# Kernel tuning notes

Measured on AMD Instinct MI355X. Metric: run time of the kernel, lower is better.

The kernel has to match this reference:

```python
import jax, jax.numpy as jnp
import numpy as np

N_HEAD = 16

def _rope(t, cos, sin):
    # t: [B,T,H,hd]; cos/sin: [T, hd//2]
    B, T, H, hd = t.shape
    tr = t.reshape(B, T, H, hd // 2, 2)
    t0, t1 = tr[..., 0], tr[..., 1]
    c = cos[None, :T, None, :]
    s = sin[None, :T, None, :]
    out = jnp.stack([t0 * c - t1 * s, t0 * s + t1 * c], axis=-1)
    return out.reshape(B, T, H, hd)

def setup_inputs() -> dict:
    key = jax.random.key(0)
    B, T, D = 2, 2048, 1024
    hd = D // N_HEAD
    ks = jax.random.split(key, 5)
    x = jax.random.normal(ks[0], (B, T, D), dtype=jnp.float32)
    Wq = jax.random.normal(ks[1], (D, D), dtype=jnp.float32) * 0.02
    Wk = jax.random.normal(ks[2], (D, D), dtype=jnp.float32) * 0.02
    Wv = jax.random.normal(ks[3], (D, D), dtype=jnp.float32) * 0.02
    Wo = jax.random.normal(ks[4], (D, D), dtype=jnp.float32) * 0.02
    # Real rotary tables (cos/sin of theta-based angles), matching precompute_freqs_cis
    theta = 10000.0
    inv_freq = 1.0 / (theta ** (np.arange(0, hd, 2, dtype=np.float32) / hd))
    ang = np.outer(np.arange(T, dtype=np.float32), inv_freq)  # [T, hd//2]
    freqs_cos = jnp.asarray(np.cos(ang), dtype=jnp.float32)
    freqs_sin = jnp.asarray(np.sin(ang), dtype=jnp.float32)
    return {"x": x, "Wq": Wq, "Wk": Wk, "Wv": Wv, "Wo": Wo,
            "freqs_cos": freqs_cos, "freqs_sin": freqs_sin}

def reference(x, Wq, Wk, Wv, Wo, freqs_cos, freqs_sin):
    B, T, D = x.shape
    H = N_HEAD
    hd = D // H
    scale = hd ** -0.5
    q = (x @ Wq.T).reshape(B, T, H, hd)
    k = (x @ Wk.T).reshape(B, T, H, hd)
    v = (x @ Wv.T).reshape(B, T, H, hd)
    q = _rope(q, freqs_cos, freqs_sin)
    k = _rope(k, freqs_cos, freqs_sin)
    # scores: [B,H,T,T]
    scores = jnp.einsum('bqhd,bkhd->bhqk', q, k) * scale
    causal = jnp.tril(jnp.ones((T, T), dtype=bool))
    scores = jnp.where(causal[None, None], scores, -jnp.inf)
    attn = jax.nn.softmax(scores, axis=-1)
    out = jnp.einsum('bhqk,bkhd->bqhd', attn, v).reshape(B, T, D)
    return out @ Wo.T
```

## Files before the change

kernel.cpp:

```cpp
#include <hip/hip_runtime.h>
#include <math.h>

typedef __bf16 bf16;
typedef __bf16 bf16x8 __attribute__((ext_vector_type(8)));
typedef __bf16 bf16x4 __attribute__((ext_vector_type(4)));
typedef __bf16 bf16x2 __attribute__((ext_vector_type(2)));
typedef float  f32x4  __attribute__((ext_vector_type(4)));

#define B_DIM 2
#define T_LEN 2048
#define D_DIM 1024
#define N_HEAD 16
#define HEAD_D 64
#define M_ROWS (B_DIM * T_LEN)

#define GLDS16(g, l)                                                          \
    __builtin_amdgcn_global_load_lds(                                         \
        (const __attribute__((address_space(1))) void*)(g),                   \
        (__attribute__((address_space(3))) void*)(l), 16, 0, 0)

__global__ void prep_cvt(const float* __restrict__ x, const float* __restrict__ wq,
                         const float* __restrict__ wk, const float* __restrict__ wv,
                         const float* __restrict__ wo, bf16* __restrict__ xb,
                         bf16* __restrict__ wqkv, bf16* __restrict__ wob) {
    int id = blockIdx.x * blockDim.x + threadIdx.x;
    if (id >= (1 << 21)) return;
    const float* src; bf16* dst; int off;
    if (id < (1 << 20)) { src = x; dst = xb; off = id; }
    else {
        int r = id - (1 << 20);
        int wi = r >> 18;
        off = r & ((1 << 18) - 1);
        src = wi == 0 ? wq : wi == 1 ? wk : wi == 2 ? wv : wo;
        dst = wi < 3 ? wqkv + ((size_t)wi << 20) : wob;
    }
    float4 v = reinterpret_cast<const float4*>(src)[off];
    bf16x4 w;
    w[0] = (bf16)v.x; w[1] = (bf16)v.y; w[2] = (bf16)v.z; w[3] = (bf16)v.w;
    reinterpret_cast<bf16x4*>(dst)[off] = w;
}

template <int MODE>
__global__ __launch_bounds__(256)
void gemm_glds(const bf16* __restrict__ A, const bf16* __restrict__ Bm,
               bf16* __restrict__ q, bf16* __restrict__ k, bf16* __restrict__ v,
               float* __restrict__ outf) {
    constexpr int K = D_DIM;
    __shared__ bf16 As[128 * 64];
    __shared__ bf16 Bs[128 * 64];
    const int tid = threadIdx.x, lane = tid & 63, wave = tid >> 6;
    const int wr = wave >> 1, wc = wave & 1;
    const int rowg = lane >> 4, col0 = lane & 15;

    const int nwg = gridDim.x * gridDim.y, cpx = nwg >> 3;
    const int lin = blockIdx.x + blockIdx.y * gridDim.x;
    const int nid = (lin & 7) * cpx + (lin >> 3);
    const int bx = nid % gridDim.x, by = nid / gridDim.x;
    const int m0 = by * 128, n0 = bx * 128;

    const int srow = lane >> 3;
    const int schk = (lane & 7) ^ srow;
    const bf16* gA = A + (size_t)(m0 + wave * 32 + srow) * K + schk * 8;
    const bf16* gB = Bm + (size_t)(n0 + wave * 32 + srow) * K + schk * 8;

    f32x4 acc[4][4];
    f32x4 zero = {0.f, 0.f, 0.f, 0.f};
#pragma unroll
    for (int i = 0; i < 4; i++)
#pragma unroll
        for (int j = 0; j < 4; j++) acc[i][j] = zero;

    for (int k0 = 0; k0 < K; k0 += 64) {
#pragma unroll
        for (int t = 0; t < 4; ++t) {
            GLDS16(gA + k0 + t * 8 * K, &As[(wave * 32 + t * 8) * 64]);
            GLDS16(gB + k0 + t * 8 * K, &Bs[(wave * 32 + t * 8) * 64]);
        }
        __syncthreads();
#pragma unroll
        for (int kk = 0; kk < 2; ++kk) {
            bf16x8 af[4], bfr[4];
#pragma unroll
            for (int i = 0; i < 4; i++) {
                int R = wr * 64 + i * 16 + col0;
                af[i] = *reinterpret_cast<const bf16x8*>(&As[R * 64 + (((kk * 4 + rowg) ^ (R & 7)) * 8)]);
            }
#pragma unroll
            for (int j = 0; j < 4; j++) {
                int R = wc * 64 + j * 16 + col0;
                bfr[j] = *reinterpret_cast<const bf16x8*>(&Bs[R * 64 + (((kk * 4 + rowg) ^ (R & 7)) * 8)]);
            }
#pragma unroll
            for (int i = 0; i < 4; i++)
#pragma unroll
                for (int j = 0; j < 4; j++)
                    acc[i][j] = __builtin_amdgcn_mfma_f32_16x16x32_bf16(af[i], bfr[j], acc[i][j], 0, 0, 0);
        }
        __syncthreads();
    }

    if constexpr (MODE == 0) {
        const int which = bx >> 3;
        if (which < 2) {
            bf16* dst = which == 0 ? q : k;
#pragma unroll
            for (int i = 0; i < 4; i++)
#pragma unroll
                for (int j = 0; j < 4; j++)
#pragma unroll
                    for (int r = 0; r < 4; r++) {
                        int m = m0 + wr * 64 + i * 16 + rowg * 4 + r;
                        int n = (n0 + wc * 64 + j * 16 + col0) & 1023;
                        int b = m >> 11, t = m & 2047, h = n >> 6, d = n & 63;
                        dst[(((size_t)(b * N_HEAD + h)) * T_LEN + t) * HEAD_D + d] = (bf16)acc[i][j][r];
                    }
        } else {
#pragma unroll
            for (int i = 0; i < 4; i++)
#pragma unroll
                for (int j = 0; j < 4; j++) {
                    bf16x4 pk;
#pragma unroll
                    for (int r = 0; r < 4; r++) pk[r] = (bf16)acc[i][j][r];
                    int m = m0 + wr * 64 + i * 16 + rowg * 4;
                    int n = (n0 + wc * 64 + j * 16 + col0) & 1023;
                    int b = m >> 11, t = m & 2047, h = n >> 6, d = n & 63;
                    *reinterpret_cast<bf16x4*>(
                        &v[(((size_t)(b * N_HEAD + h)) * HEAD_D + d) * T_LEN + t]) = pk;
                }
        }
    } else {
#pragma unroll
        for (int i = 0; i < 4; i++)
#pragma unroll
            for (int j = 0; j < 4; j++)
#pragma unroll
                for (int r = 0; r < 4; r++) {
                    int m = m0 + wr * 64 + i * 16 + rowg * 4 + r;
                    int n = n0 + wc * 64 + j * 16 + col0;
                    outf[(size_t)m * D_DIM + n] = acc[i][j][r];
                }
    }
}

__global__ void rope_inplace(bf16* __restrict__ q, bf16* __restrict__ k,
                             const float* __restrict__ cosT, const float* __restrict__ sinT) {
    int id = blockIdx.x * blockDim.x + threadIdx.x;
    int i = id & 31;
    int t = (id >> 5) & 2047;
    int bh = id >> 16;
    float c = cosT[t * 32 + i], s = sinT[t * 32 + i];
    size_t p = ((size_t)bh * T_LEN + t) * HEAD_D + 2 * i;
    float q0 = (float)q[p], q1 = (float)q[p + 1];
    q[p]     = (bf16)((q0 * c - q1 * s) * 0.125f);
    q[p + 1] = (bf16)((q0 * s + q1 * c) * 0.125f);
    float k0 = (float)k[p], k1 = (float)k[p + 1];
    k[p]     = (bf16)(k0 * c - k1 * s);
    k[p + 1] = (bf16)(k0 * s + k1 * c);
}

__global__ __launch_bounds__(512)
void attn_fwd(const bf16* __restrict__ qh, const bf16* __restrict__ kh,
              const bf16* __restrict__ vtg, bf16* __restrict__ ao) {
    __shared__ __align__(16) bf16 Ks[2][64 * 64];
    __shared__ __align__(16) bf16 Vs[2][64 * 64];
    __shared__ __align__(16) bf16 Ps[8][16][72];
    const int tid = threadIdx.x, lane = tid & 63, w = tid >> 6;
    const int g = lane >> 4, q15 = lane & 15;
    const int lin = blockIdx.x + blockIdx.y * 8;
    const int nid = (lin & 7) * 32 + (lin >> 3);
    const int pi = nid & 7, bh = nid >> 3;
    const size_t kbase = (size_t)bh * T_LEN * HEAD_D;
    const size_t vbase = (size_t)bh * HEAD_D * T_LEN;
    const int srow = tid >> 3, scg = tid & 7;
    const int sel = srow * 64 + ((scg * 8) ^ ((srow & 7) * 8));
    const int ksw = (q15 & 7) * 8;

    const float NEGINF = -__builtin_inff();
    f32x4 zero = {0.f, 0.f, 0.f, 0.f};

    for (int ph = 0; ph < 2; ++ph) {
        const int qi = ph ? (15 - pi) : pi;
        const int q0 = qi * 128;
        const int nt = 2 * qi + 2;
        const int qlo = q0 + w * 16;

        bf16x8 aq[2];
#pragma unroll
        for (int kk = 0; kk < 2; ++kk)
            aq[kk] = *reinterpret_cast<const bf16x8*>(
                &qh[kbase + (size_t)(qlo + q15) * HEAD_D + kk * 32 + g * 8]);

        f32x4 o[4];
#pragma unroll
        for (int j = 0; j < 4; j++) o[j] = zero;
        float mi = NEGINF, li = 0.f;

        {
            uint4 kr = *reinterpret_cast<const uint4*>(&kh[kbase + (size_t)srow * HEAD_D + scg * 8]);
            uint4 vr = *reinterpret_cast<const uint4*>(&vtg[vbase + (size_t)srow * T_LEN + scg * 8]);
            *reinterpret_cast<uint4*>(&Ks[0][sel]) = kr;
            *reinterpret_cast<uint4*>(&Vs[0][sel]) = vr;
        }
        __syncthreads();

        for (int kt = 0; kt < nt; ++kt) {
            const int cur = kt & 1;
            const int kv0 = kt * 64;
            const bool pf = (kt + 1 < nt);
            uint4 kr, vr;
            if (pf) {
                kr = *reinterpret_cast<const uint4*>(&kh[kbase + (size_t)(kv0 + 64 + srow) * HEAD_D + scg * 8]);
                vr = *reinterpret_cast<const uint4*>(&vtg[vbase + (size_t)srow * T_LEN + kv0 + 64 + scg * 8]);
            }

            f32x4 sT[4];
#pragma unroll
            for (int j = 0; j < 4; j++) sT[j] = zero;
            __builtin_amdgcn_s_setprio(1);
#pragma unroll
            for (int kk = 0; kk < 2; ++kk) {
                const int ko = (kk * 32 + g * 8) ^ ksw;
#pragma unroll
                for (int j = 0; j < 4; j++) {
                    bf16x8 bk = *reinterpret_cast<const bf16x8*>(&Ks[cur][(j * 16 + q15) * 64 + ko]);
                    sT[j] = __builtin_amdgcn_mfma_f32_16x16x32_bf16(bk, aq[kk], sT[j], 0, 0, 0);
                }
            }
            __builtin_amdgcn_s_setprio(0);
            if (kv0 + 63 > qlo) {
                const int qg = qlo + q15;
#pragma unroll
                for (int j = 0; j < 4; j++)
#pragma unroll
                    for (int r = 0; r < 4; r++)
                        if (kv0 + j * 16 + g * 4 + r > qg) sT[j][r] = NEGINF;
            }
            float mx = sT[0][0];
#pragma unroll
            for (int j = 0; j < 4; j++)
#pragma unroll
                for (int r = 0; r < 4; r++) mx = fmaxf(mx, sT[j][r]);
            mx = fmaxf(mx, __shfl_xor(mx, 16));
            mx = fmaxf(mx, __shfl_xor(mx, 32));
            const float mnew = fmaxf(mi, mx);
            const float al = __expf(mi - mnew);
            float ps = 0.f;
#pragma unroll
            for (int j = 0; j < 4; j++)
#pragma unroll
                for (int r = 0; r < 4; r++) {
                    float p = __expf(sT[j][r] - mnew);
                    sT[j][r] = p;
                    ps += p;
                }
            ps += __shfl_xor(ps, 16);
            ps += __shfl_xor(ps, 32);
            li = li * al + ps;
            mi = mnew;
#pragma unroll
            for (int j = 0; j < 4; j++)
#pragma unroll
                for (int pr = 0; pr < 2; ++pr) {
                    bf16x2 pk;
                    pk[0] = (bf16)sT[j][2 * pr];
                    pk[1] = (bf16)sT[j][2 * pr + 1];
                    *reinterpret_cast<bf16x2*>(&Ps[w][q15][j * 16 + g * 4 + 2 * pr]) = pk;
                }
#pragma unroll
            for (int j = 0; j < 4; j++)
#pragma unroll
                for (int r = 0; r < 4; r++) o[j][r] *= al;
            __builtin_amdgcn_s_setprio(1);
#pragma unroll
            for (int kk = 0; kk < 2; ++kk) {
                bf16x8 pb = *reinterpret_cast<const bf16x8*>(&Ps[w][q15][kk * 32 + g * 8]);
                const int ko = (kk * 32 + g * 8) ^ ksw;
#pragma unroll
                for (int j = 0; j < 4; j++) {
                    bf16x8 av = *reinterpret_cast<const bf16x8*>(&Vs[cur][(j * 16 + q15) * 64 + ko]);
                    o[j] = __builtin_amdgcn_mfma_f32_16x16x32_bf16(av, pb, o[j], 0, 0, 0);
                }
            }
            __builtin_amdgcn_s_setprio(0);
            if (pf) {
                *reinterpret_cast<uint4*>(&Ks[cur ^ 1][sel]) = kr;
                *reinterpret_cast<uint4*>(&Vs[cur ^ 1][sel]) = vr;
            }
            __syncthreads();
        }

        const int b = bh >> 4, h = bh & 15;
        const float inv = 1.f / li;
        const int t = qlo + q15;
        bf16* dst = &ao[((size_t)(b * T_LEN + t)) * D_DIM + h * HEAD_D];
#pragma unroll
        for (int j = 0; j < 4; j++) {
            bf16x4 pk;
#pragma unroll
            for (int r = 0; r < 4; r++) pk[r] = (bf16)(o[j][r] * inv);
            *reinterpret_cast<bf16x4*>(&dst[j * 16 + g * 4]) = pk;
        }
    }
}

extern "C" void kernel_launch(void* const* d_in, const int* in_sizes, int n_in,
                              void* d_out, int out_size, void* d_ws, size_t ws_size,
                              hipStream_t stream) {
    const float* x  = (const float*)d_in[0];
    const float* Wq = (const float*)d_in[1];
    const float* Wk = (const float*)d_in[2];
    const float* Wv = (const float*)d_in[3];
    const float* Wo = (const float*)d_in[4];
    const float* fc = (const float*)d_in[5];
    const float* fs = (const float*)d_in[6];
    float* out = (float*)d_out;

    char* ws = (char*)d_ws;
    const size_t MB = 1024 * 1024;
    bf16* xb   = (bf16*)(ws);
    bf16* wqkv = (bf16*)(ws + 8 * MB);
    bf16* wob  = (bf16*)(ws + 14 * MB);
    bf16* qhd  = (bf16*)(ws + 16 * MB);
    bf16* khd  = (bf16*)(ws + 24 * MB);
    bf16* vt   = (bf16*)(ws + 32 * MB);
    bf16* ao   = (bf16*)(ws + 40 * MB);

    prep_cvt<<<8192, 256, 0, stream>>>(x, Wq, Wk, Wv, Wo, xb, wqkv, wob);

    dim3 gq(24, 32);
    gemm_glds<0><<<gq, 256, 0, stream>>>(xb, wqkv, qhd, khd, vt, nullptr);

    rope_inplace<<<(B_DIM * N_HEAD * T_LEN * 32) / 256, 256, 0, stream>>>(qhd, khd, fc, fs);

    dim3 ga(8, B_DIM * N_HEAD);
    attn_fwd<<<ga, 512, 0, stream>>>(qhd, khd, vt, ao);

    dim3 go(8, 32);
    gemm_glds<1><<<go, 256, 0, stream>>>(ao, wob, nullptr, nullptr, nullptr, out);
}
```

Before: 119.8 us.

## Fuse RoPE into attention, double-buffer GEMM LDS, shrink attention blocks

Result: slower. 134.8 us (+12.6%).

```diff
diff --git a/kernel.cpp b/kernel.cpp
--- a/kernel.cpp
+++ b/kernel.cpp
@@ -41,13 +41,13 @@
 }
 
 template <int MODE>
-__global__ __launch_bounds__(256)
+__global__ __launch_bounds__(256, 2)
 void gemm_glds(const bf16* __restrict__ A, const bf16* __restrict__ Bm,
                bf16* __restrict__ q, bf16* __restrict__ k, bf16* __restrict__ v,
                float* __restrict__ outf) {
     constexpr int K = D_DIM;
-    __shared__ bf16 As[128 * 64];
-    __shared__ bf16 Bs[128 * 64];
+    __shared__ bf16 As[2][128 * 64];
+    __shared__ bf16 Bs[2][128 * 64];
     const int tid = threadIdx.x, lane = tid & 63, wave = tid >> 6;
     const int wr = wave >> 1, wc = wave & 1;
     const int rowg = lane >> 4, col0 = lane & 15;
@@ -70,31 +70,47 @@
 #pragma unroll
         for (int j = 0; j < 4; j++) acc[i][j] = zero;
 
-    for (int k0 = 0; k0 < K; k0 += 64) {
-#pragma unroll
-        for (int t = 0; t < 4; ++t) {
-            GLDS16(gA + k0 + t * 8 * K, &As[(wave * 32 + t * 8) * 64]);
-            GLDS16(gB + k0 + t * 8 * K, &Bs[(wave * 32 + t * 8) * 64]);
-        }
-        __syncthreads();
+#pragma unroll
+    for (int t = 0; t < 4; ++t) {
+        GLDS16(gA + t * 8 * K, &As[0][(wave * 32 + t * 8) * 64]);
+        GLDS16(gB + t * 8 * K, &Bs[0][(wave * 32 + t * 8) * 64]);
+    }
+    __syncthreads();
+
+    for (int kt = 0; kt < 16; ++kt) {
+        const int cur = kt & 1;
+        const bool pf = (kt + 1 < 16);
+        const int knext = (kt + 1) * 64;
+        if (pf) {
+#pragma unroll
+            for (int t = 0; t < 4; ++t)
+                GLDS16(gA + knext + t * 8 * K, &As[cur ^ 1][(wave * 32 + t * 8) * 64]);
+        }
 #pragma unroll
         for (int kk = 0; kk < 2; ++kk) {
             bf16x8 af[4], bfr[4];
 #pragma unroll
             for (int i = 0; i < 4; i++) {
                 int R = wr * 64 + i * 16 + col0;
-                af[i] = *reinterpret_cast<const bf16x8*>(&As[R * 64 + (((kk * 4 + rowg) ^ (R & 7)) * 8)]);
+                af[i] = *reinterpret_cast<const bf16x8*>(&As[cur][R * 64 + (((kk * 4 + rowg) ^ (R & 7)) * 8)]);
             }
 #pragma unroll
             for (int j = 0; j < 4; j++) {
                 int R = wc * 64 + j * 16 + col0;
-                bfr[j] = *reinterpret_cast<const bf16x8*>(&Bs[R * 64 + (((kk * 4 + rowg) ^ (R & 7)) * 8)]);
-            }
+                bfr[j] = *reinterpret_cast<const bf16x8*>(&Bs[cur][R * 64 + (((kk * 4 + rowg) ^ (R & 7)) * 8)]);
+            }
+            __builtin_amdgcn_s_setprio(1);
 #pragma unroll
             for (int i = 0; i < 4; i++)
 #pragma unroll
                 for (int j = 0; j < 4; j++)
                     acc[i][j] = __builtin_amdgcn_mfma_f32_16x16x32_bf16(af[i], bfr[j], acc[i][j], 0, 0, 0);
+            __builtin_amdgcn_s_setprio(0);
+            if (kk == 0 && pf) {
+#pragma unroll
+                for (int t = 0; t < 4; ++t)
+                    GLDS16(gB + knext + t * 8 * K, &Bs[cur ^ 1][(wave * 32 + t * 8) * 64]);
+            }
         }
         __syncthreads();
     }
@@ -143,53 +159,54 @@
     }
 }
 
-__global__ void rope_inplace(bf16* __restrict__ q, bf16* __restrict__ k,
-                             const float* __restrict__ cosT, const float* __restrict__ sinT) {
-    int id = blockIdx.x * blockDim.x + threadIdx.x;
-    int i = id & 31;
-    int t = (id >> 5) & 2047;
-    int bh = id >> 16;
-    float c = cosT[t * 32 + i], s = sinT[t * 32 + i];
-    size_t p = ((size_t)bh * T_LEN + t) * HEAD_D + 2 * i;
-    float q0 = (float)q[p], q1 = (float)q[p + 1];
-    q[p]     = (bf16)((q0 * c - q1 * s) * 0.125f);
-    q[p + 1] = (bf16)((q0 * s + q1 * c) * 0.125f);
-    float k0 = (float)k[p], k1 = (float)k[p + 1];
-    k[p]     = (bf16)(k0 * c - k1 * s);
-    k[p + 1] = (bf16)(k0 * s + k1 * c);
-}
-
-__global__ __launch_bounds__(512)
+__device__ inline bf16x8 rope8(bf16x8 v, f32x4 c4, f32x4 s4, float scale) {
+    bf16x8 r;
+#pragma unroll
+    for (int m = 0; m < 4; ++m) {
+        float a = (float)v[2 * m], b = (float)v[2 * m + 1];
+        r[2 * m]     = (bf16)((a * c4[m] - b * s4[m]) * scale);
+        r[2 * m + 1] = (bf16)((a * s4[m] + b * c4[m]) * scale);
+    }
+    return r;
+}
+
+__global__ __launch_bounds__(256, 2)
 void attn_fwd(const bf16* __restrict__ qh, const bf16* __restrict__ kh,
-              const bf16* __restrict__ vtg, bf16* __restrict__ ao) {
+              const bf16* __restrict__ vtg, const float* __restrict__ fc,
+              const float* __restrict__ fs, bf16* __restrict__ ao) {
     __shared__ __align__(16) bf16 Ks[2][64 * 64];
     __shared__ __align__(16) bf16 Vs[2][64 * 64];
-    __shared__ __align__(16) bf16 Ps[8][16][72];
+    __shared__ __align__(16) bf16 Ps[4][16][72];
     const int tid = threadIdx.x, lane = tid & 63, w = tid >> 6;
     const int g = lane >> 4, q15 = lane & 15;
-    const int lin = blockIdx.x + blockIdx.y * 8;
-    const int nid = (lin & 7) * 32 + (lin >> 3);
-    const int pi = nid & 7, bh = nid >> 3;
+    const int lin = blockIdx.x + blockIdx.y * 16;
+    const int nid = (lin & 7) * 64 + (lin >> 3);
+    const int pi = nid & 15, bh = nid >> 4;
     const size_t kbase = (size_t)bh * T_LEN * HEAD_D;
     const size_t vbase = (size_t)bh * HEAD_D * T_LEN;
-    const int srow = tid >> 3, scg = tid & 7;
-    const int sel = srow * 64 + ((scg * 8) ^ ((srow & 7) * 8));
+    const int c0row = tid >> 3, ccg = tid & 7;
+    const int swz = (ccg * 8) ^ ((c0row & 7) * 8);
+    const int sel0 = c0row * 64 + swz;
+    const int sel1 = sel0 + 32 * 64;
     const int ksw = (q15 & 7) * 8;
 
     const float NEGINF = -__builtin_inff();
     f32x4 zero = {0.f, 0.f, 0.f, 0.f};
 
     for (int ph = 0; ph < 2; ++ph) {
-        const int qi = ph ? (15 - pi) : pi;
-        const int q0 = qi * 128;
-        const int nt = 2 * qi + 2;
-        const int qlo = q0 + w * 16;
+        const int qi = ph ? (31 - pi) : pi;
+        const int nt = qi + 1;
+        const int qlo = qi * 64 + w * 16;
 
         bf16x8 aq[2];
 #pragma unroll
-        for (int kk = 0; kk < 2; ++kk)
-            aq[kk] = *reinterpret_cast<const bf16x8*>(
+        for (int kk = 0; kk < 2; ++kk) {
+            bf16x8 qv = *reinterpret_cast<const bf16x8*>(
                 &qh[kbase + (size_t)(qlo + q15) * HEAD_D + kk * 32 + g * 8]);
+            f32x4 c4 = *reinterpret_cast<const f32x4*>(&fc[(qlo + q15) * 32 + kk * 16 + g * 4]);
+            f32x4 s4 = *reinterpret_cast<const f32x4*>(&fs[(qlo + q15) * 32 + kk * 16 + g * 4]);
+            aq[kk] = rope8(qv, c4, s4, 0.125f);
+        }
 
         f32x4 o[4];
 #pragma unroll
@@ -197,10 +214,18 @@
         float mi = NEGINF, li = 0.f;
 
         {
-            uint4 kr = *reinterpret_cast<const uint4*>(&kh[kbase + (size_t)srow * HEAD_D + scg * 8]);
-            uint4 vr = *reinterpret_cast<const uint4*>(&vtg[vbase + (size_t)srow * T_LEN + scg * 8]);
-            *reinterpret_cast<uint4*>(&Ks[0][sel]) = kr;
-            *reinterpret_cast<uint4*>(&Vs[0][sel]) = vr;
+            bf16x8 k80 = *reinterpret_cast<const bf16x8*>(&kh[kbase + (size_t)c0row * HEAD_D + ccg * 8]);
+            bf16x8 k81 = *reinterpret_cast<const bf16x8*>(&kh[kbase + (size_t)(c0row + 32) * HEAD_D + ccg * 8]);
+            f32x4 c40 = *reinterpret_cast<const f32x4*>(&fc[c0row * 32 + ccg * 4]);
+            f32x4 s40 = *reinterpret_cast<const f32x4*>(&fs[c0row * 32 + ccg * 4]);
+            f32x4 c41 = *reinterpret_cast<const f32x4*>(&fc[(c0row + 32) * 32 + ccg * 4]);
+            f32x4 s41 = *reinterpret_cast<const f32x4*>(&fs[(c0row + 32) * 32 + ccg * 4]);
+            bf16x8 v80 = *reinterpret_cast<const bf16x8*>(&vtg[vbase + (size_t)c0row * T_LEN + ccg * 8]);
+            bf16x8 v81 = *reinterpret_cast<const bf16x8*>(&vtg[vbase + (size_t)(c0row + 32) * T_LEN + ccg * 8]);
+            *reinterpret_cast<bf16x8*>(&Ks[0][sel0]) = rope8(k80, c40, s40, 1.f);
+            *reinterpret_cast<bf16x8*>(&Ks[0][sel1]) = rope8(k81, c41, s41, 1.f);
+            *reinterpret_cast<bf16x8*>(&Vs[0][sel0]) = v80;
+            *reinterpret_cast<bf16x8*>(&Vs[0][sel1]) = v81;
         }
         __syncthreads();
 
@@ -208,10 +233,18 @@
             const int cur = kt & 1;
             const int kv0 = kt * 64;
             const bool pf = (kt + 1 < nt);
-            uint4 kr, vr;
+            bf16x8 k80, k81, v80, v81;
+            f32x4 c40, s40, c41, s41;
             if (pf) {
-                kr = *reinterpret_cast<const uint4*>(&kh[kbase + (size_t)(kv0 + 64 + srow) * HEAD_D + scg * 8]);
-                vr = *reinterpret_cast<const uint4*>(&vtg[vbase + (size_t)srow * T_LEN + kv0 + 64 + scg * 8]);
+                const int kn = kv0 + 64;
+                k80 = *reinterpret_cast<const bf16x8*>(&kh[kbase + (size_t)(kn + c0row) * HEAD_D + ccg * 8]);
+                k81 = *reinterpret_cast<const bf16x8*>(&kh[kbase + (size_t)(kn + c0row + 32) * HEAD_D + ccg * 8]);
+                c40 = *reinterpret_cast<const f32x4*>(&fc[(kn + c0row) * 32 + ccg * 4]);
+                s40 = *reinterpret_cast<const f32x4*>(&fs[(kn + c0row) * 32 + ccg * 4]);
+                c41 = *reinterpret_cast<const f32x4*>(&fc[(kn + c0row + 32) * 32 + ccg * 4]);
+                s41 = *reinterpret_cast<const f32x4*>(&fs[(kn + c0row + 32) * 32 + ccg * 4]);
+                v80 = *reinterpret_cast<const bf16x8*>(&vtg[vbase + (size_t)c0row * T_LEN + kn + ccg * 8]);
+                v81 = *reinterpret_cast<const bf16x8*>(&vtg[vbase + (size_t)(c0row + 32) * T_LEN + kn + ccg * 8]);
             }
 
             f32x4 sT[4];
@@ -284,8 +317,10 @@
             }
             __builtin_amdgcn_s_setprio(0);
             if (pf) {
-                *reinterpret_cast<uint4*>(&Ks[cur ^ 1][sel]) = kr;
-                *reinterpret_cast<uint4*>(&Vs[cur ^ 1][sel]) = vr;
+                *reinterpret_cast<bf16x8*>(&Ks[cur ^ 1][sel0]) = rope8(k80, c40, s40, 1.f);
+                *reinterpret_cast<bf16x8*>(&Ks[cur ^ 1][sel1]) = rope8(k81, c41, s41, 1.f);
+                *reinterpret_cast<bf16x8*>(&Vs[cur ^ 1][sel0]) = v80;
+                *reinterpret_cast<bf16x8*>(&Vs[cur ^ 1][sel1]) = v81;
             }
             __syncthreads();
         }
@@ -331,10 +366,8 @@
     dim3 gq(24, 32);
     gemm_glds<0><<<gq, 256, 0, stream>>>(xb, wqkv, qhd, khd, vt, nullptr);
 
-    rope_inplace<<<(B_DIM * N_HEAD * T_LEN * 32) / 256, 256, 0, stream>>>(qhd, khd, fc, fs);
-
-    dim3 ga(8, B_DIM * N_HEAD);
-    attn_fwd<<<ga, 512, 0, stream>>>(qhd, khd, vt, ao);
+    dim3 ga(16, B_DIM * N_HEAD);
+    attn_fwd<<<ga, 256, 0, stream>>>(qhd, khd, vt, fc, fs, ao);
 
     dim3 go(8, 32);
     gemm_glds<1><<<go, 256, 0, stream>>>(ao, wob, nullptr, nullptr, nullptr, out);
```
